# Performance work log

Measured on AMD Instinct MI355X. Metric: run time of the kernel, lower is better.

Reference implementation:

```python
import jax, jax.numpy as jnp
import numpy as np

L = 32768          # sequence length (keys/values)
E = 1024           # embed_dim (hardcoded in module via weight slices)
H, D = 8, 128      # num_heads, head_dim (hardcoded via reshape(-1, 8, 128))


def setup_inputs() -> dict:
    key = jax.random.key(0)
    k1, k2, k3, k4, k5 = jax.random.split(key, 5)
    scale = 1.0 / np.sqrt(E)
    return {
        "x": jax.random.normal(k1, (L, E), dtype=jnp.float32),
        "in_proj_weight": jax.random.normal(k2, (3 * E, E), dtype=jnp.float32) * scale,
        "in_proj_bias": jax.random.normal(k3, (3 * E,), dtype=jnp.float32) * 0.02,
        "out_proj_weight": jax.random.normal(k4, (E, E), dtype=jnp.float32) * scale,
        "out_proj_bias": jax.random.normal(k5, (E,), dtype=jnp.float32) * 0.02,
    }


def reference(x, in_proj_weight, in_proj_bias, out_proj_weight, out_proj_bias):
    # Single-query (decode-style) attention: q from first token only.
    q = x[:1] @ in_proj_weight[:E].T + in_proj_bias[:E]              # [1, E]
    k = x @ in_proj_weight[E:2 * E].T + in_proj_bias[E:2 * E]        # [L, E]
    v = x @ in_proj_weight[2 * E:].T + in_proj_bias[2 * E:]          # [L, E]

    q = q.reshape(-1, H, D).transpose(1, 0, 2)                       # [H, 1, D]
    k = k.reshape(-1, H, D).transpose(1, 2, 0)                       # [H, D, L]
    v = v.reshape(-1, H, D).transpose(1, 0, 2)                       # [H, L, D]

    dot = jnp.matmul(q, k) * (1.0 / np.sqrt(D))                      # [H, 1, L]
    attn = jax.nn.softmax(dot, axis=-1)
    out = jnp.matmul(attn, v)                                        # [H, 1, D]

    out = out.transpose(1, 0, 2).reshape(-1, E)                      # [1, E]
    out = out @ out_proj_weight.T + out_proj_bias                    # [1, E]
    return out
```

## Files before the change

### kernel.cpp

```cpp
#include <hip/hip_runtime.h>
#include <math.h>


#define L_SEQ   32768
#define E_DIM   1024
#define NHEAD   8
#define HDIM    128
#define NBLK    256

#define GLD16(gp, lp)                                                   \
  __builtin_amdgcn_global_load_lds(                                     \
      (const __attribute__((address_space(1))) void*)(gp),              \
      (__attribute__((address_space(3))) void*)(lp), 16, 0, 0)

__device__ __forceinline__ void gbar(int* bar, int phase)
{
  __syncthreads();
  if (threadIdx.x == 0) {
    __threadfence();
    int* cnt  = bar + ((blockIdx.x & 7) << 5);
    int* lvl2 = bar + 256;
    int* rel  = bar + 320;
    bool last = false;
    if (__hip_atomic_fetch_add(cnt, 1, __ATOMIC_RELAXED,
                               __HIP_MEMORY_SCOPE_AGENT) == 31) {
      if (__hip_atomic_fetch_add(lvl2, 1, __ATOMIC_RELAXED,
                                 __HIP_MEMORY_SCOPE_AGENT) == 7) {
        __threadfence();
#pragma unroll
        for (int i = 0; i < 8; ++i)
          __hip_atomic_store(bar + (i << 5), 0, __ATOMIC_RELAXED,
                             __HIP_MEMORY_SCOPE_AGENT);
        __hip_atomic_store(lvl2, 0, __ATOMIC_RELAXED, __HIP_MEMORY_SCOPE_AGENT);
        __hip_atomic_store(rel, phase, __ATOMIC_RELEASE,
                           __HIP_MEMORY_SCOPE_AGENT);
        last = true;
      }
    }
    if (!last) {
      while (__hip_atomic_load(rel, __ATOMIC_RELAXED,
                               __HIP_MEMORY_SCOPE_AGENT) < phase)
        __builtin_amdgcn_s_sleep(4);
    }
    __threadfence();
  }
  __syncthreads();
}

__global__ __launch_bounds__(512, 1) void mha_all(
    const float* __restrict__ x,   const float* __restrict__ Wi,
    const float* __restrict__ bi,  const float* __restrict__ Wo,
    const float* __restrict__ bo,  float* __restrict__ out,
    float* __restrict__ P_T, float* __restrict__ zn,
    float* __restrict__ attn, float* __restrict__ psumw,
    float* __restrict__ pz, int* bar)
{
  __shared__ __align__(16) float smem[8 * 4 * E_DIM];
  __shared__ __align__(16) float swq[32];
  __shared__ __align__(16) float swst4[8][NHEAD];
  __shared__ float sumw_s[NHEAD];

  const int t    = threadIdx.x;
  const int wave = t >> 6;
  const int lane = t & 63;
  const int bid  = blockIdx.x;

  if (bid < NHEAD) {
    const int h = bid;
    float* q_lds = smem;

    float4 x0[4];
    {
      const float4* xr0 = (const float4*)x;
#pragma unroll
      for (int c = 0; c < 4; ++c) x0[c] = xr0[64 * c + lane];
    }
#pragma unroll
    for (int i = 0; i < 16; ++i) {
      const int op = wave * 16 + i;
      const int o  = h * HDIM + op;
      const float4* Wr = (const float4*)(Wi + (size_t)o * E_DIM);
      float a = 0.f;
#pragma unroll
      for (int c = 0; c < 4; ++c) {
        float4 wv = Wr[64 * c + lane];
        a += wv.x * x0[c].x + wv.y * x0[c].y + wv.z * x0[c].z + wv.w * x0[c].w;
      }
#pragma unroll
      for (int m = 1; m < 64; m <<= 1) a += __shfl_xor(a, m, 64);
      if (lane == 0) q_lds[op] = a + bi[o];
    }
    __syncthreads();

    float acc0 = 0.f, acc1 = 0.f;
    const float* Wk = Wi + ((size_t)E_DIM + (size_t)h * HDIM) * E_DIM;
#pragma unroll 4
    for (int d = 0; d < HDIM; ++d) {
      const float qv = q_lds[d];
      const float2 wv = *(const float2*)(Wk + (size_t)d * E_DIM + 2 * t);
      acc0 += qv * wv.x; acc1 += qv * wv.y;
    }
    const float sc = 0.08838834764831845f;
    *(float2*)(P_T + (size_t)h * E_DIM + 2 * t) = make_float2(acc0 * sc, acc1 * sc);
    __syncthreads();
  }
  gbar(bar, 1);

  {
    const int hq = wave & 1;
    const int rg = wave >> 1;
    const size_t row0 = (size_t)bid * (L_SEQ / NBLK);

    float4 p[4][4];
#pragma unroll
    for (int j = 0; j < 4; ++j) {
      const float4* P0 = (const float4*)(P_T + (size_t)(4 * hq + j) * E_DIM);
#pragma unroll
      for (int c = 0; c < 4; ++c) p[j][c] = P0[64 * c + lane];
    }

    float4 z[4][4];
#pragma unroll
    for (int j = 0; j < 4; ++j)
#pragma unroll
      for (int c = 0; c < 4; ++c) z[j][c] = make_float4(0.f, 0.f, 0.f, 0.f);
    float sumw[4] = {0.f, 0.f, 0.f, 0.f};

    float4 xa[4], xb[4];
    {
      const float4* g0 = (const float4*)(x + (row0 + rg) * E_DIM);
      const float4* g1 = (const float4*)(x + (row0 + rg + 4) * E_DIM);
#pragma unroll
      for (int c = 0; c < 4; ++c) { xa[c] = g0[64 * c + lane]; xb[c] = g1[64 * c + lane]; }
    }

#pragma unroll 2
    for (int k = 0; k < 32; ++k) {
      float4 xn[4];
      if (k < 30) {
        const float4* g = (const float4*)(x + (row0 + rg + 4 * (k + 2)) * E_DIM);
#pragma unroll
        for (int c = 0; c < 4; ++c) xn[c] = g[64 * c + lane];
      }

      float s[4] = {0.f, 0.f, 0.f, 0.f};
#pragma unroll
      for (int j = 0; j < 4; ++j)
#pragma unroll
        for (int c = 0; c < 4; ++c)
          s[j] += xa[c].x * p[j][c].x + xa[c].y * p[j][c].y +
                  xa[c].z * p[j][c].z + xa[c].w * p[j][c].w;

#pragma unroll
      for (int m = 1; m < 64; m <<= 1) {
#pragma unroll
        for (int j = 0; j < 4; ++j) s[j] += __shfl_xor(s[j], m, 64);
      }

      float w[4];
#pragma unroll
      for (int j = 0; j < 4; ++j) { w[j] = __expf(s[j]); sumw[j] += w[j]; }

#pragma unroll
      for (int j = 0; j < 4; ++j)
#pragma unroll
        for (int c = 0; c < 4; ++c) {
          z[j][c].x += w[j] * xa[c].x; z[j][c].y += w[j] * xa[c].y;
          z[j][c].z += w[j] * xa[c].z; z[j][c].w += w[j] * xa[c].w;
        }

#pragma unroll
      for (int c = 0; c < 4; ++c) { xa[c] = xb[c]; xb[c] = xn[c]; }
    }

    {
      float4* zd = (float4*)(smem + wave * 4096);
#pragma unroll
      for (int j = 0; j < 4; ++j)
#pragma unroll
        for (int c = 0; c < 4; ++c) zd[j * 256 + 64 * c + lane] = z[j][c];
      if (lane == 0) {
#pragma unroll
        for (int j = 0; j < 4; ++j) swq[wave * 4 + j] = sumw[j];
      }
    }
    __syncthreads();
    {
      float* pzb = pz + (size_t)bid * (NHEAD * E_DIM);
#pragma unroll
      for (int m = 0; m < 16; ++m) {
        const int idx = t + 512 * m;
        const int h  = idx >> 10;
        const int e  = idx & 1023;
        const int hh = h >> 2;
        const int j  = h & 3;
        float v = 0.f;
#pragma unroll
        for (int rg2 = 0; rg2 < 4; ++rg2)
          v += smem[(2 * rg2 + hh) * 4096 + j * 1024 + e];
        pzb[idx] = v;
      }
    }
    if (t < NHEAD) {
      const int hh = t >> 2, j = t & 3;
      float s2 = 0.f;
#pragma unroll
      for (int rg2 = 0; rg2 < 4; ++rg2) s2 += swq[(2 * rg2 + hh) * 4 + j];
      psumw[bid * NHEAD + t] = s2;
    }
  }
  gbar(bar, 2);

  {
    float* red = smem;
    float sw[NHEAD];
#pragma unroll
    for (int h = 0; h < NHEAD; ++h) sw[h] = 0.f;
    for (int b2 = t; b2 < NBLK; b2 += 512) {
      const float4* p = (const float4*)(psumw + (size_t)b2 * NHEAD);
      float4 a0 = p[0], a1 = p[1];
      sw[0] += a0.x; sw[1] += a0.y; sw[2] += a0.z; sw[3] += a0.w;
      sw[4] += a1.x; sw[5] += a1.y; sw[6] += a1.z; sw[7] += a1.w;
    }
#pragma unroll
    for (int m = 1; m < 64; m <<= 1) {
#pragma unroll
      for (int h = 0; h < NHEAD; ++h) sw[h] += __shfl_xor(sw[h], m, 64);
    }
    if (lane == 0) {
#pragma unroll
      for (int h = 0; h < NHEAD; ++h) swst4[wave][h] = sw[h];
    }
    __syncthreads();
    if (t < NHEAD) {
      float s = 0.f;
#pragma unroll
      for (int wv = 0; wv < 8; ++wv) s += swst4[wv][t];
      sumw_s[t] = s;
    }

    const int o = bid * 32 + (t & 31);
    const int g = t >> 5;
    float a = 0.f;
    for (int b2 = g; b2 < NBLK; b2 += 16) a += pz[(size_t)b2 * (NHEAD * E_DIM) + o];
    red[t] = a;
    __syncthreads();
    if (t < 32) {
      float s2 = 0.f;
#pragma unroll
      for (int gg = 0; gg < 16; ++gg) s2 += red[gg * 32 + t];
      const int oo = bid * 32 + t;
      zn[oo] = s2 / sumw_s[oo >> 10];
    }
  }
  gbar(bar, 3);

  if (bid < 128) {
    const int o = bid * 8 + wave;
    const float4* Wr = (const float4*)(Wi + ((size_t)2 * E_DIM + o) * E_DIM);
    const float4* zr = (const float4*)(zn + (size_t)(o >> 7) * E_DIM);
    float a = 0.f;
#pragma unroll
    for (int k = 0; k < 4; ++k) {
      float4 wv = Wr[lane + 64 * k];
      float4 zv = zr[lane + 64 * k];
      a += wv.x * zv.x + wv.y * zv.y + wv.z * zv.z + wv.w * zv.w;
    }
#pragma unroll
    for (int m = 1; m < 64; m <<= 1) a += __shfl_xor(a, m, 64);
    if (lane == 0) attn[o] = a + bi[2 * E_DIM + o];
  }
  gbar(bar, 4);

  if (bid < 128) {
    const int o = bid * 8 + wave;
    const float4* Wr = (const float4*)(Wo + (size_t)o * E_DIM);
    const float4* vr = (const float4*)attn;
    float a = 0.f;
#pragma unroll
    for (int k = 0; k < 4; ++k) {
      float4 wv = Wr[lane + 64 * k];
      float4 vv = vr[lane + 64 * k];
      a += wv.x * vv.x + wv.y * vv.y + wv.z * vv.z + wv.w * vv.w;
    }
#pragma unroll
    for (int m = 1; m < 64; m <<= 1) a += __shfl_xor(a, m, 64);
    if (lane == 0) out[o] = a + bo[o];
  }
}


__global__ __launch_bounds__(256) void proj_q(
    const float* __restrict__ W, const float* __restrict__ bias,
    const float* __restrict__ x, float* __restrict__ q)
{
  const int t = threadIdx.x, wave = t >> 6, lane = t & 63;
  const int o = blockIdx.x * 4 + wave;
  const float4* Wr = (const float4*)(W + (size_t)o * E_DIM);
  const float4* xr = (const float4*)x;
  float a = 0.f;
#pragma unroll
  for (int k = 0; k < 4; ++k) {
    float4 wv = Wr[lane + 64 * k];
    float4 xv = xr[lane + 64 * k];
    a += wv.x * xv.x + wv.y * xv.y + wv.z * xv.z + wv.w * xv.w;
  }
#pragma unroll
  for (int m = 1; m < 64; m <<= 1) a += __shfl_xor(a, m, 64);
  if (lane == 0) q[o] = a + bias[o];
}

__global__ __launch_bounds__(128) void make_p(
    const float* __restrict__ W, const float* __restrict__ q,
    float* __restrict__ P_T)
{
  const int h = blockIdx.y;
  const int e = blockIdx.x * 128 + threadIdx.x;
  const float* qh = q + h * HDIM;
  const float* Wb = W + ((size_t)E_DIM + (size_t)h * HDIM) * E_DIM + e;
  float a0 = 0.f, a1 = 0.f, a2 = 0.f, a3 = 0.f;
#pragma unroll 4
  for (int d = 0; d < HDIM; d += 4) {
    a0 += qh[d + 0] * Wb[(size_t)(d + 0) * E_DIM];
    a1 += qh[d + 1] * Wb[(size_t)(d + 1) * E_DIM];
    a2 += qh[d + 2] * Wb[(size_t)(d + 2) * E_DIM];
    a3 += qh[d + 3] * Wb[(size_t)(d + 3) * E_DIM];
  }
  P_T[h * E_DIM + e] = ((a0 + a1) + (a2 + a3)) * 0.08838834764831845f;
}

__global__ __launch_bounds__(512, 2) void attn_fused5(
    const float* __restrict__ x, const float* __restrict__ P_T,
    float* __restrict__ partial_z, float* __restrict__ partial_sumw,
    int rows_per_blk)
{
  __shared__ __align__(16) float sbuf[2][8][E_DIM];
  __shared__ float swst[16];
  const int t = threadIdx.x, wave = t >> 6, lane = t & 63;
  const int rh = wave >> 2, h0 = (wave & 3) * 2;
  const size_t row0 = (size_t)blockIdx.x * rows_per_blk;
  const int ntiles = rows_per_blk / 8;

  float4 p0[4], p1[4];
  {
    const float4* P0 = (const float4*)(P_T + (size_t)h0 * E_DIM);
    const float4* P1 = (const float4*)(P_T + (size_t)(h0 + 1) * E_DIM);
#pragma unroll
    for (int k = 0; k < 4; ++k) { p0[k] = P0[64 * k + lane]; p1[k] = P1[64 * k + lane]; }
  }
  float4 z0[4], z1[4];
#pragma unroll
  for (int k = 0; k < 4; ++k) {
    z0[k] = make_float4(0.f, 0.f, 0.f, 0.f);
    z1[k] = make_float4(0.f, 0.f, 0.f, 0.f);
  }
  float sumw0 = 0.f, sumw1 = 0.f;
  {
    const float* g = x + (row0 + wave) * E_DIM + 4 * lane;
#pragma unroll
    for (int k = 0; k < 4; ++k) GLD16(g + k * 256, &sbuf[0][wave][k * 256]);
  }
  __syncthreads();
  for (int tile = 0; tile < ntiles; ++tile) {
    const int buf = tile & 1;
    if (tile + 1 < ntiles) {
      const float* g = x + (row0 + (size_t)(tile + 1) * 8 + wave) * E_DIM + 4 * lane;
#pragma unroll
      for (int k = 0; k < 4; ++k) GLD16(g + k * 256, &sbuf[buf ^ 1][wave][k * 256]);
    }
#pragma unroll
    for (int rl = 0; rl < 4; ++rl) {
      const float4* xr4 = (const float4*)&sbuf[buf][rh * 4 + rl][0];
      float4 xr[4];
#pragma unroll
      for (int k = 0; k < 4; ++k) xr[k] = xr4[64 * k + lane];
      float s0 = 0.f, s1 = 0.f;
#pragma unroll
      for (int k = 0; k < 4; ++k) {
        s0 += xr[k].x * p0[k].x + xr[k].y * p0[k].y + xr[k].z * p0[k].z + xr[k].w * p0[k].w;
        s1 += xr[k].x * p1[k].x + xr[k].y * p1[k].y + xr[k].z * p1[k].z + xr[k].w * p1[k].w;
      }
      const bool odd = (lane & 1);
      float keep = odd ? s1 : s0;
      float oth  = odd ? s0 : s1;
      float ts = keep + __shfl_xor(oth, 1, 64);
      ts += __shfl_xor(ts, 2, 64);
      ts += __shfl_xor(ts, 4, 64);
      ts += __shfl_xor(ts, 8, 64);
      ts += __shfl_xor(ts, 16, 64);
      ts += __shfl_xor(ts, 32, 64);
      const float ex = __expf(ts);
      const float ox = __shfl_xor(ex, 1, 64);
      const float w0 = odd ? ox : ex;
      const float w1 = odd ? ex : ox;
      sumw0 += w0; sumw1 += w1;
#pragma unroll
      for (int k = 0; k < 4; ++k) {
        z0[k].x += w0 * xr[k].x; z0[k].y += w0 * xr[k].y;
        z0[k].z += w0 * xr[k].z; z0[k].w += w0 * xr[k].w;
        z1[k].x += w1 * xr[k].x; z1[k].y += w1 * xr[k].y;
        z1[k].z += w1 * xr[k].z; z1[k].w += w1 * xr[k].w;
      }
    }
    __syncthreads();
  }
  float (*zs)[E_DIM] = (float(*)[E_DIM])&sbuf[0][0][0];
  {
    float4* zd0 = (float4*)&zs[2 * wave][0];
    float4* zd1 = (float4*)&zs[2 * wave + 1][0];
#pragma unroll
    for (int k = 0; k < 4; ++k) { zd0[64 * k + lane] = z0[k]; zd1[64 * k + lane] = z1[k]; }
  }
  if (lane == 0) { swst[2 * wave] = sumw0; swst[2 * wave + 1] = sumw1; }
  __syncthreads();
  {
    const float4* zsv = (const float4*)&zs[0][0];
    float4* pzb = (float4*)(partial_z + (size_t)blockIdx.x * (NHEAD * E_DIM));
#pragma unroll
    for (int j = 0; j < 4; ++j) {
      const int idx = t + 512 * j;
      const float4 a = zsv[idx], b = zsv[idx + 2048];
      pzb[idx] = make_float4(a.x + b.x, a.y + b.y, a.z + b.z, a.w + b.w);
    }
  }
  if (t < NHEAD)
    partial_sumw[blockIdx.x * NHEAD + t] = swst[t] + swst[t + 8];
}

__global__ __launch_bounds__(256) void reduce_z(
    const float* __restrict__ partial_z, const float* __restrict__ partial_sumw,
    float* __restrict__ zn, int nblk)
{
  __shared__ float red[256];
  __shared__ __align__(16) float swst[4][NHEAD];
  __shared__ float sumw_s[NHEAD];
  const int t = threadIdx.x;
  const int lane = t & 63, wave = t >> 6;
  float sw[NHEAD];
#pragma unroll
  for (int h = 0; h < NHEAD; ++h) sw[h] = 0.f;
  for (int b = t; b < nblk; b += 256) {
    const float4* p = (const float4*)(partial_sumw + (size_t)b * NHEAD);
    float4 a0 = p[0], a1 = p[1];
    sw[0] += a0.x; sw[1] += a0.y; sw[2] += a0.z; sw[3] += a0.w;
    sw[4] += a1.x; sw[5] += a1.y; sw[6] += a1.z; sw[7] += a1.w;
  }
#pragma unroll
  for (int m = 1; m < 64; m <<= 1) {
#pragma unroll
    for (int h = 0; h < NHEAD; ++h) sw[h] += __shfl_xor(sw[h], m, 64);
  }
  if (lane == 0) {
#pragma unroll
    for (int h = 0; h < NHEAD; ++h) swst[wave][h] = sw[h];
  }
  __syncthreads();
  if (t < NHEAD) sumw_s[t] = swst[0][t] + swst[1][t] + swst[2][t] + swst[3][t];
  const int o = blockIdx.x * 32 + (t & 31);
  const int g = t >> 5;
  float a = 0.f;
  for (int b = g; b < nblk; b += 8) a += partial_z[(size_t)b * (NHEAD * E_DIM) + o];
  red[t] = a;
  __syncthreads();
  if (t < 32) {
    float s2 = 0.f;
#pragma unroll
    for (int gg = 0; gg < 8; ++gg) s2 += red[gg * 32 + t];
    const int oo = blockIdx.x * 32 + t;
    zn[oo] = s2 / sumw_s[oo >> 10];
  }
}

__global__ __launch_bounds__(256) void proj_v(
    const float* __restrict__ W, const float* __restrict__ bias,
    const float* __restrict__ zn, float* __restrict__ attn)
{
  const int t = threadIdx.x, wave = t >> 6, lane = t & 63;
  const int o = blockIdx.x * 4 + wave;
  const float4* Wr = (const float4*)(W + ((size_t)2 * E_DIM + o) * E_DIM);
  const float4* zr = (const float4*)(zn + (size_t)(o >> 7) * E_DIM);
  float a = 0.f;
#pragma unroll
  for (int k = 0; k < 4; ++k) {
    float4 wv = Wr[lane + 64 * k];
    float4 zv = zr[lane + 64 * k];
    a += wv.x * zv.x + wv.y * zv.y + wv.z * zv.z + wv.w * zv.w;
  }
#pragma unroll
  for (int m = 1; m < 64; m <<= 1) a += __shfl_xor(a, m, 64);
  if (lane == 0) attn[o] = a + bias[2 * E_DIM + o];
}

__global__ __launch_bounds__(256) void proj_o(
    const float* __restrict__ Wo, const float* __restrict__ bo,
    const float* __restrict__ attn, float* __restrict__ out)
{
  const int t = threadIdx.x, wave = t >> 6, lane = t & 63;
  const int o = blockIdx.x * 4 + wave;
  const float4* Wr = (const float4*)(Wo + (size_t)o * E_DIM);
  const float4* vr = (const float4*)attn;
  float a = 0.f;
#pragma unroll
  for (int k = 0; k < 4; ++k) {
    float4 wv = Wr[lane + 64 * k];
    float4 vv = vr[lane + 64 * k];
    a += wv.x * vv.x + wv.y * vv.y + wv.z * vv.z + wv.w * vv.w;
  }
#pragma unroll
  for (int m = 1; m < 64; m <<= 1) a += __shfl_xor(a, m, 64);
  if (lane == 0) out[o] = a + bo[o];
}

extern "C" void kernel_launch(void* const* d_in, const int* in_sizes, int n_in,
                              void* d_out, int out_size, void* d_ws, size_t ws_size,
                              hipStream_t stream)
{
  const float* x  = (const float*)d_in[0];
  const float* Wi = (const float*)d_in[1];
  const float* bi = (const float*)d_in[2];
  const float* Wo = (const float*)d_in[3];
  const float* bo = (const float*)d_in[4];
  float* out = (float*)d_out;

  char* ws = (char*)d_ws;
  float* q     = (float*)(ws + 0);
  float* P_T   = (float*)(ws + 4096);
  float* zn    = (float*)(ws + 36864);
  float* attn  = (float*)(ws + 69632);
  float* psumw = (float*)(ws + 73728);
  int*   bar   = (int*)  (ws + 81920);
  const size_t pz_off = 90112;
  float* pz    = (float*)(ws + pz_off);

  const size_t need_coop = pz_off + (size_t)NBLK * NHEAD * E_DIM * 4;
  if (ws_size >= need_coop) {
    hipMemsetAsync(bar, 0, 2048, stream);
    mha_all<<<NBLK, 512, 0, stream>>>(x, Wi, bi, Wo, bo, out,
                                      P_T, zn, attn, psumw, pz, bar);
    return;
  }

  int nblk = 128;
  if (ws_size >= pz_off + (size_t)512 * NHEAD * E_DIM * 4) nblk = 512;
  else if (ws_size >= pz_off + (size_t)256 * NHEAD * E_DIM * 4) nblk = 256;
  const int rows_per_blk = L_SEQ / nblk;

  proj_q     <<<256, 256, 0, stream>>>(Wi, bi, x, q);
  make_p     <<<dim3(8, 8), 128, 0, stream>>>(Wi, q, P_T);
  attn_fused5<<<nblk, 512, 0, stream>>>(x, P_T, pz, psumw, rows_per_blk);
  reduce_z   <<<256, 256, 0, stream>>>(pz, psumw, zn, nblk);
  proj_v     <<<256, 256, 0, stream>>>(Wi, bi, zn, attn);
  proj_o     <<<256, 256, 0, stream>>>(Wo, bo, attn, out);
}
```

Before: 299.9 us.

## Spread q/P projection over all blocks and rebalance row and output mapping

```diff
diff --git a/kernel.cpp b/kernel.cpp
--- a/kernel.cpp
+++ b/kernel.cpp
@@ -40,7 +40,7 @@
     if (!last) {
       while (__hip_atomic_load(rel, __ATOMIC_RELAXED,
                                __HIP_MEMORY_SCOPE_AGENT) < phase)
-        __builtin_amdgcn_s_sleep(4);
+        __builtin_amdgcn_s_sleep(1);
     }
     __threadfence();
   }
@@ -65,51 +65,55 @@
   const int lane = t & 63;
   const int bid  = blockIdx.x;
 
-  if (bid < NHEAD) {
-    const int h = bid;
+  {
+    const int h  = bid >> 5;
+    const int ec = bid & 31;
     float* q_lds = smem;
-
-    float4 x0[4];
+    float (*ps)[32] = (float(*)[32])(smem + 256);
+
     {
-      const float4* xr0 = (const float4*)x;
-#pragma unroll
-      for (int c = 0; c < 4; ++c) x0[c] = xr0[64 * c + lane];
-    }
-#pragma unroll
-    for (int i = 0; i < 16; ++i) {
-      const int op = wave * 16 + i;
-      const int o  = h * HDIM + op;
-      const float4* Wr = (const float4*)(Wi + (size_t)o * E_DIM);
+      const int d   = t >> 2;
+      const int sub = t & 3;
+      const float4* W4 = (const float4*)(Wi + (size_t)(h * HDIM + d) * E_DIM + sub * 256);
+      const float4* X4 = (const float4*)(x + sub * 256);
       float a = 0.f;
-#pragma unroll
-      for (int c = 0; c < 4; ++c) {
-        float4 wv = Wr[64 * c + lane];
-        a += wv.x * x0[c].x + wv.y * x0[c].y + wv.z * x0[c].z + wv.w * x0[c].w;
-      }
-#pragma unroll
-      for (int m = 1; m < 64; m <<= 1) a += __shfl_xor(a, m, 64);
-      if (lane == 0) q_lds[op] = a + bi[o];
-    }
-    __syncthreads();
-
-    float acc0 = 0.f, acc1 = 0.f;
-    const float* Wk = Wi + ((size_t)E_DIM + (size_t)h * HDIM) * E_DIM;
-#pragma unroll 4
-    for (int d = 0; d < HDIM; ++d) {
-      const float qv = q_lds[d];
-      const float2 wv = *(const float2*)(Wk + (size_t)d * E_DIM + 2 * t);
-      acc0 += qv * wv.x; acc1 += qv * wv.y;
-    }
-    const float sc = 0.08838834764831845f;
-    *(float2*)(P_T + (size_t)h * E_DIM + 2 * t) = make_float2(acc0 * sc, acc1 * sc);
+#pragma unroll 8
+      for (int j = 0; j < 64; ++j) {
+        const float4 wv = W4[j], xv = X4[j];
+        a += wv.x * xv.x + wv.y * xv.y + wv.z * xv.z + wv.w * xv.w;
+      }
+      a += __shfl_xor(a, 1, 64);
+      a += __shfl_xor(a, 2, 64);
+      if (sub == 0) q_lds[d] = a + bi[h * HDIM + d];
+    }
+    __syncthreads();
+
+    {
+      const int dg  = t >> 5;
+      const int cl  = t & 31;
+      const int col = ec * 32 + cl;
+      const float* Wk = Wi + ((size_t)E_DIM + h * HDIM + dg * 8) * E_DIM + col;
+      float a = 0.f;
+#pragma unroll
+      for (int i = 0; i < 8; ++i)
+        a += q_lds[dg * 8 + i] * Wk[(size_t)i * E_DIM];
+      ps[dg][cl] = a;
+    }
+    __syncthreads();
+    if (t < 32) {
+      float s = 0.f;
+#pragma unroll
+      for (int g = 0; g < 16; ++g) s += ps[g][t];
+      P_T[(size_t)h * E_DIM + ec * 32 + t] = s * 0.08838834764831845f;
+    }
     __syncthreads();
   }
   gbar(bar, 1);
 
   {
-    const int hq = wave & 1;
-    const int rg = wave >> 1;
-    const size_t row0 = (size_t)bid * (L_SEQ / NBLK);
+    const int hq   = wave & 1;
+    const int rgrp = wave >> 1;
+    const size_t row0 = (size_t)bid * 128 + (size_t)rgrp * 32;
 
     float4 p[4][4];
 #pragma unroll
@@ -128,8 +132,8 @@
 
     float4 xa[4], xb[4];
     {
-      const float4* g0 = (const float4*)(x + (row0 + rg) * E_DIM);
-      const float4* g1 = (const float4*)(x + (row0 + rg + 4) * E_DIM);
+      const float4* g0 = (const float4*)(x + row0 * E_DIM);
+      const float4* g1 = (const float4*)(x + (row0 + 1) * E_DIM);
 #pragma unroll
       for (int c = 0; c < 4; ++c) { xa[c] = g0[64 * c + lane]; xb[c] = g1[64 * c + lane]; }
     }
@@ -138,7 +142,7 @@
     for (int k = 0; k < 32; ++k) {
       float4 xn[4];
       if (k < 30) {
-        const float4* g = (const float4*)(x + (row0 + rg + 4 * (k + 2)) * E_DIM);
+        const float4* g = (const float4*)(x + (row0 + k + 2) * E_DIM);
 #pragma unroll
         for (int c = 0; c < 4; ++c) xn[c] = g[64 * c + lane];
       }
@@ -255,8 +259,8 @@
   }
   gbar(bar, 3);
 
-  if (bid < 128) {
-    const int o = bid * 8 + wave;
+  if (wave < 4) {
+    const int o = bid * 4 + wave;
     const float4* Wr = (const float4*)(Wi + ((size_t)2 * E_DIM + o) * E_DIM);
     const float4* zr = (const float4*)(zn + (size_t)(o >> 7) * E_DIM);
     float a = 0.f;
@@ -272,8 +276,8 @@
   }
   gbar(bar, 4);
 
-  if (bid < 128) {
-    const int o = bid * 8 + wave;
+  if (wave < 4) {
+    const int o = bid * 4 + wave;
     const float4* Wr = (const float4*)(Wo + (size_t)o * E_DIM);
     const float4* vr = (const float4*)attn;
     float a = 0.f;
```

After: 286.2 us. -4.6%, faster.
